# Kernel optimization log

Hardware: AMD Instinct MI355X
Metric: run time of the kernel (lower is better)

## Reference

```python
import jax, jax.numpy as jnp
import numpy as np

D0 = 1.0          # constraint distance d
NPEND = 128       # points per pendulum chain
NB = 1024         # number of chains (= batch.max()+1)
LATENT = 256      # latent dim of y
NDIM = 3          # spatial dimensions; x dim = 2*NDIM (pos + vel)


def setup_inputs() -> dict:
    key = jax.random.key(0)
    k1, k2, k3 = jax.random.split(key, 3)
    N = NB * NPEND
    y = jax.random.normal(k1, (N, LATENT), dtype=jnp.float32)
    z = jax.random.normal(k2, (N,), dtype=jnp.float32)
    K = jax.random.normal(k3, (LATENT, 2 * NDIM), dtype=jnp.float32) * 0.05
    batch = (jnp.arange(N, dtype=jnp.int32) // NPEND).astype(jnp.int32)
    return {"y": y, "z": z, "K": K, "batch": batch}


def _delta_r(r):
    # dr[:,0] = r[:,0]; dr[:,i] = r[:,i] - r[:,i-1]
    return jnp.concatenate([r[:, :1], r[:, 1:] - r[:, :-1]], axis=1)


def reference(y, z, K, batch):
    x = y @ K                                  # [N, 6]
    ndim = x.shape[-1] // 2                    # pos_only=False -> 3
    nb = batch.shape[0] // NPEND               # == batch.max()+1 by construction
    r = x[:, :ndim].reshape(nb, -1, ndim)      # [nb, npend, 3]

    dr = _delta_r(r)                           # [nb, npend, 3]
    drnorm = jnp.linalg.norm(dr, axis=-1)      # [nb, npend]
    c = drnorm - D0                            # constraint values
    rn = dr / drnorm[..., None]                # unit chain-difference vectors

    # Jacobian-transpose times constraints, fused over the chain dimension:
    # out[:,i] = c_i * rn_i - c_{i+1} * rn_{i+1};  out[:,-1] = c_{-1} * rn_{-1}
    t = c[..., None] * rn                      # [nb, npend, 3]
    out = t - jnp.concatenate([t[:, 1:], jnp.zeros_like(t[:, :1])], axis=1)

    lam_x = jnp.zeros_like(x).at[:, :ndim].set(out.reshape(-1, ndim))
    lam_y = lam_x @ K.T                        # [N, latent]
    return lam_y
```

## Files before the change

kernel.cpp:

```cpp
#include <hip/hip_runtime.h>

#define NPEND  128
#define LATENT 256
#define KCOLS  6
#define D0_C   1.0f
#define SEG    32
#define SEGS_PER_CHAIN (NPEND / SEG)
#define ROWS_PER_HALF 5

__global__ __launch_bounds__(256, 4)
void pend_kernel_f32(const float* __restrict__ y,
                     const float* __restrict__ K,
                     float* __restrict__ out)
{
    __shared__ float sKT[3][LATENT];
    __shared__ float sR[SEG + 2][3];

    const int tid  = threadIdx.x;
    const int hwid = tid >> 5;
    const int hl   = tid & 31;

    const int chain = blockIdx.x >> 2;
    const int seg   = blockIdx.x & 3;
    const int row0  = seg * SEG;
    const int rlo   = (row0 > 0) ? row0 - 1 : 0;
    const int rhi   = (row0 + SEG < NPEND) ? row0 + SEG : NPEND - 1;
    const int nrows = rhi - rlo + 1;

    {
        const float ka = K[tid * KCOLS + 0];
        const float kb = K[tid * KCOLS + 1];
        const float kc = K[tid * KCOLS + 2];
        sKT[0][tid] = ka;
        sKT[1][tid] = kb;
        sKT[2][tid] = kc;
    }
    __syncthreads();

    const size_t cbase = (size_t)chain * ((size_t)NPEND * LATENT);
    const int l0 = hl * 4;

    float4 va[ROWS_PER_HALF], vb[ROWS_PER_HALF];
#pragma unroll
    for (int j = 0; j < ROWS_PER_HALF; ++j) {
        int i = hwid + 8 * j;
        int row = rlo + ((i < nrows) ? i : (nrows - 1));
        const float* yr = y + cbase + (size_t)row * LATENT;
        va[j] = *(const float4*)(yr + l0);
        vb[j] = *(const float4*)(yr + 128 + l0);
    }

    const float4 k0a = *(const float4*)&sKT[0][l0];
    const float4 k0b = *(const float4*)&sKT[0][l0 + 128];
    const float4 k1a = *(const float4*)&sKT[1][l0];
    const float4 k1b = *(const float4*)&sKT[1][l0 + 128];
    const float4 k2a = *(const float4*)&sKT[2][l0];
    const float4 k2b = *(const float4*)&sKT[2][l0 + 128];

    __builtin_amdgcn_sched_barrier(0);

    float s0[ROWS_PER_HALF], s1[ROWS_PER_HALF], s2[ROWS_PER_HALF];
#pragma unroll
    for (int j = 0; j < ROWS_PER_HALF; ++j) {
        s0[j] = va[j].x*k0a.x + va[j].y*k0a.y + va[j].z*k0a.z + va[j].w*k0a.w
              + vb[j].x*k0b.x + vb[j].y*k0b.y + vb[j].z*k0b.z + vb[j].w*k0b.w;
        s1[j] = va[j].x*k1a.x + va[j].y*k1a.y + va[j].z*k1a.z + va[j].w*k1a.w
              + vb[j].x*k1b.x + vb[j].y*k1b.y + vb[j].z*k1b.z + vb[j].w*k1b.w;
        s2[j] = va[j].x*k2a.x + va[j].y*k2a.y + va[j].z*k2a.z + va[j].w*k2a.w
              + vb[j].x*k2b.x + vb[j].y*k2b.y + vb[j].z*k2b.z + vb[j].w*k2b.w;
    }

#pragma unroll
    for (int off = 16; off > 0; off >>= 1) {
#pragma unroll
        for (int j = 0; j < ROWS_PER_HALF; ++j) {
            s0[j] += __shfl_down(s0[j], off, 32);
            s1[j] += __shfl_down(s1[j], off, 32);
            s2[j] += __shfl_down(s2[j], off, 32);
        }
    }
    if (hl == 0) {
#pragma unroll
        for (int j = 0; j < ROWS_PER_HALF; ++j) {
            int i = hwid + 8 * j;
            if (i < nrows) {
                sR[i][0] = s0[j]; sR[i][1] = s1[j]; sR[i][2] = s2[j];
            }
        }
    }
    __syncthreads();

#pragma unroll
    for (int j = 0; j < SEG / 8; ++j) {
        const int i   = hwid + 8 * j;
        const int row = row0 + i;
        const int si  = row - rlo;

        const float rx = sR[si][0], ry = sR[si][1], rz = sR[si][2];
        float px = 0.f, py = 0.f, pz = 0.f;
        if (row > 0) { px = sR[si-1][0]; py = sR[si-1][1]; pz = sR[si-1][2]; }

        const float dx = rx - px, dy = ry - py, dz = rz - pz;
        const float n  = sqrtf(dx*dx + dy*dy + dz*dz);
        const float s  = (n - D0_C) / n;
        float ox = s * dx, oy = s * dy, oz = s * dz;

        if (row < NPEND - 1) {
            const float nx = sR[si+1][0], ny = sR[si+1][1], nz = sR[si+1][2];
            const float ex = nx - rx, ey = ny - ry, ez = nz - rz;
            const float n2 = sqrtf(ex*ex + ey*ey + ez*ez);
            const float t2 = (n2 - D0_C) / n2;
            ox -= t2 * ex; oy -= t2 * ey; oz -= t2 * ez;
        }

        float4 wa, wb;
        wa.x = ox*k0a.x + oy*k1a.x + oz*k2a.x;
        wa.y = ox*k0a.y + oy*k1a.y + oz*k2a.y;
        wa.z = ox*k0a.z + oy*k1a.z + oz*k2a.z;
        wa.w = ox*k0a.w + oy*k1a.w + oz*k2a.w;
        wb.x = ox*k0b.x + oy*k1b.x + oz*k2b.x;
        wb.y = ox*k0b.y + oy*k1b.y + oz*k2b.y;
        wb.z = ox*k0b.z + oy*k1b.z + oz*k2b.z;
        wb.w = ox*k0b.w + oy*k1b.w + oz*k2b.w;

        float* orow = out + cbase + (size_t)row * LATENT;
        *(float4*)(orow + l0)       = wa;
        *(float4*)(orow + 128 + l0) = wb;
    }
}

extern "C" void kernel_launch(void* const* d_in, const int* in_sizes, int n_in,
                              void* d_out, int out_size, void* d_ws, size_t ws_size,
                              hipStream_t stream) {
    const float* y = (const float*)d_in[0];
    const float* K = (const float*)d_in[2];
    float* out = (float*)d_out;

    int N  = (n_in > 1 && in_sizes) ? in_sizes[1] : (1024 * NPEND);
    int nb = N / NPEND;
    if (nb <= 0) nb = 1024;
    (void)out_size; (void)d_ws; (void)ws_size;

    pend_kernel_f32<<<nb * SEGS_PER_CHAIN, 256, 0, stream>>>(y, K, out);
}
```

Baseline: 236.0 us.

## Process whole chain per block with double-buffered segment loads

Each block now handles an entire 128-row chain instead of a 32-row segment, which removes the halo rows that were re-read from y at segment boundaries. Loads for the next segment are issued while the current segment is reduced, and each segment's output is written one iteration later so loads, reductions and stores overlap. Stores become nontemporal. In exchange the grid shrinks to 1024 blocks, which lowers parallelism, and register pressure rises from the double-buffered loads.

```diff
diff --git a/kernel.cpp b/kernel.cpp
--- a/kernel.cpp
+++ b/kernel.cpp
@@ -5,8 +5,10 @@
 #define KCOLS  6
 #define D0_C   1.0f
 #define SEG    32
-#define SEGS_PER_CHAIN (NPEND / SEG)
-#define ROWS_PER_HALF 5
+#define NSEG   (NPEND / SEG)
+#define JROWS  4
+
+typedef float f32x4 __attribute__((ext_vector_type(4)));
 
 __global__ __launch_bounds__(256, 4)
 void pend_kernel_f32(const float* __restrict__ y,
@@ -14,18 +16,15 @@
                      float* __restrict__ out)
 {
     __shared__ float sKT[3][LATENT];
-    __shared__ float sR[SEG + 2][3];
+    __shared__ float sR[NPEND][3];
 
     const int tid  = threadIdx.x;
     const int hwid = tid >> 5;
     const int hl   = tid & 31;
+    const int l0   = hl * 4;
 
-    const int chain = blockIdx.x >> 2;
-    const int seg   = blockIdx.x & 3;
-    const int row0  = seg * SEG;
-    const int rlo   = (row0 > 0) ? row0 - 1 : 0;
-    const int rhi   = (row0 + SEG < NPEND) ? row0 + SEG : NPEND - 1;
-    const int nrows = rhi - rlo + 1;
+    const int chain = blockIdx.x;
+    const size_t cbase = (size_t)chain * ((size_t)NPEND * LATENT);
 
     {
         const float ka = K[tid * KCOLS + 0];
@@ -37,19 +36,6 @@
     }
     __syncthreads();
 
-    const size_t cbase = (size_t)chain * ((size_t)NPEND * LATENT);
-    const int l0 = hl * 4;
-
-    float4 va[ROWS_PER_HALF], vb[ROWS_PER_HALF];
-#pragma unroll
-    for (int j = 0; j < ROWS_PER_HALF; ++j) {
-        int i = hwid + 8 * j;
-        int row = rlo + ((i < nrows) ? i : (nrows - 1));
-        const float* yr = y + cbase + (size_t)row * LATENT;
-        va[j] = *(const float4*)(yr + l0);
-        vb[j] = *(const float4*)(yr + 128 + l0);
-    }
-
     const float4 k0a = *(const float4*)&sKT[0][l0];
     const float4 k0b = *(const float4*)&sKT[0][l0 + 128];
     const float4 k1a = *(const float4*)&sKT[1][l0];
@@ -57,76 +43,96 @@
     const float4 k2a = *(const float4*)&sKT[2][l0];
     const float4 k2b = *(const float4*)&sKT[2][l0 + 128];
 
-    __builtin_amdgcn_sched_barrier(0);
+    float4 va[2][JROWS], vb[2][JROWS];
 
-    float s0[ROWS_PER_HALF], s1[ROWS_PER_HALF], s2[ROWS_PER_HALF];
+    auto issue = [&](int s, int b) {
 #pragma unroll
-    for (int j = 0; j < ROWS_PER_HALF; ++j) {
-        s0[j] = va[j].x*k0a.x + va[j].y*k0a.y + va[j].z*k0a.z + va[j].w*k0a.w
-              + vb[j].x*k0b.x + vb[j].y*k0b.y + vb[j].z*k0b.z + vb[j].w*k0b.w;
-        s1[j] = va[j].x*k1a.x + va[j].y*k1a.y + va[j].z*k1a.z + va[j].w*k1a.w
-              + vb[j].x*k1b.x + vb[j].y*k1b.y + vb[j].z*k1b.z + vb[j].w*k1b.w;
-        s2[j] = va[j].x*k2a.x + va[j].y*k2a.y + va[j].z*k2a.z + va[j].w*k2a.w
-              + vb[j].x*k2b.x + vb[j].y*k2b.y + vb[j].z*k2b.z + vb[j].w*k2b.w;
-    }
+        for (int j = 0; j < JROWS; ++j) {
+            const int row = s * SEG + hwid + 8 * j;
+            const float* yr = y + cbase + (size_t)row * LATENT;
+            va[b][j] = *(const float4*)(yr + l0);
+            vb[b][j] = *(const float4*)(yr + 128 + l0);
+        }
+    };
 
+    auto computeR = [&](int s, int b) {
+        float s0[JROWS], s1[JROWS], s2[JROWS];
 #pragma unroll
-    for (int off = 16; off > 0; off >>= 1) {
+        for (int j = 0; j < JROWS; ++j) {
+            const float4 a = va[b][j], bb = vb[b][j];
+            s0[j] = a.x*k0a.x + a.y*k0a.y + a.z*k0a.z + a.w*k0a.w
+                  + bb.x*k0b.x + bb.y*k0b.y + bb.z*k0b.z + bb.w*k0b.w;
+            s1[j] = a.x*k1a.x + a.y*k1a.y + a.z*k1a.z + a.w*k1a.w
+                  + bb.x*k1b.x + bb.y*k1b.y + bb.z*k1b.z + bb.w*k1b.w;
+            s2[j] = a.x*k2a.x + a.y*k2a.y + a.z*k2a.z + a.w*k2a.w
+                  + bb.x*k2b.x + bb.y*k2b.y + bb.z*k2b.z + bb.w*k2b.w;
+        }
 #pragma unroll
-        for (int j = 0; j < ROWS_PER_HALF; ++j) {
-            s0[j] += __shfl_down(s0[j], off, 32);
-            s1[j] += __shfl_down(s1[j], off, 32);
-            s2[j] += __shfl_down(s2[j], off, 32);
-        }
-    }
-    if (hl == 0) {
+        for (int off = 16; off > 0; off >>= 1) {
 #pragma unroll
-        for (int j = 0; j < ROWS_PER_HALF; ++j) {
-            int i = hwid + 8 * j;
-            if (i < nrows) {
-                sR[i][0] = s0[j]; sR[i][1] = s1[j]; sR[i][2] = s2[j];
+            for (int j = 0; j < JROWS; ++j) {
+                s0[j] += __shfl_down(s0[j], off, 32);
+                s1[j] += __shfl_down(s1[j], off, 32);
+                s2[j] += __shfl_down(s2[j], off, 32);
             }
         }
+        if (hl == 0) {
+#pragma unroll
+            for (int j = 0; j < JROWS; ++j) {
+                const int row = s * SEG + hwid + 8 * j;
+                sR[row][0] = s0[j]; sR[row][1] = s1[j]; sR[row][2] = s2[j];
+            }
+        }
+    };
+
+    auto phase2 = [&](int t) {
+#pragma unroll
+        for (int j = 0; j < JROWS; ++j) {
+            const int row = t * SEG + hwid + 8 * j;
+
+            const float rx = sR[row][0], ry = sR[row][1], rz = sR[row][2];
+            float px = 0.f, py = 0.f, pz = 0.f;
+            if (row > 0) { px = sR[row-1][0]; py = sR[row-1][1]; pz = sR[row-1][2]; }
+
+            const float dx = rx - px, dy = ry - py, dz = rz - pz;
+            const float n  = sqrtf(dx*dx + dy*dy + dz*dz);
+            const float s  = (n - D0_C) / n;
+            float ox = s * dx, oy = s * dy, oz = s * dz;
+
+            if (row < NPEND - 1) {
+                const float nx = sR[row+1][0], ny = sR[row+1][1], nz = sR[row+1][2];
+                const float ex = nx - rx, ey = ny - ry, ez = nz - rz;
+                const float n2 = sqrtf(ex*ex + ey*ey + ez*ez);
+                const float t2 = (n2 - D0_C) / n2;
+                ox -= t2 * ex; oy -= t2 * ey; oz -= t2 * ez;
+            }
+
+            f32x4 wa, wb;
+            wa.x = ox*k0a.x + oy*k1a.x + oz*k2a.x;
+            wa.y = ox*k0a.y + oy*k1a.y + oz*k2a.y;
+            wa.z = ox*k0a.z + oy*k1a.z + oz*k2a.z;
+            wa.w = ox*k0a.w + oy*k1a.w + oz*k2a.w;
+            wb.x = ox*k0b.x + oy*k1b.x + oz*k2b.x;
+            wb.y = ox*k0b.y + oy*k1b.y + oz*k2b.y;
+            wb.z = ox*k0b.z + oy*k1b.z + oz*k2b.z;
+            wb.w = ox*k0b.w + oy*k1b.w + oz*k2b.w;
+
+            float* orow = out + cbase + (size_t)row * LATENT;
+            __builtin_nontemporal_store(wa, (f32x4*)(orow + l0));
+            __builtin_nontemporal_store(wb, (f32x4*)(orow + 128 + l0));
+        }
+    };
+
+    issue(0, 0);
+#pragma unroll
+    for (int s = 0; s < NSEG; ++s) {
+        if (s + 1 < NSEG) issue(s + 1, (s + 1) & 1);
+        __builtin_amdgcn_sched_barrier(0);
+        computeR(s, s & 1);
+        __syncthreads();
+        if (s > 0) phase2(s - 1);
     }
-    __syncthreads();
-
-#pragma unroll
-    for (int j = 0; j < SEG / 8; ++j) {
-        const int i   = hwid + 8 * j;
-        const int row = row0 + i;
-        const int si  = row - rlo;
-
-        const float rx = sR[si][0], ry = sR[si][1], rz = sR[si][2];
-        float px = 0.f, py = 0.f, pz = 0.f;
-        if (row > 0) { px = sR[si-1][0]; py = sR[si-1][1]; pz = sR[si-1][2]; }
-
-        const float dx = rx - px, dy = ry - py, dz = rz - pz;
-        const float n  = sqrtf(dx*dx + dy*dy + dz*dz);
-        const float s  = (n - D0_C) / n;
-        float ox = s * dx, oy = s * dy, oz = s * dz;
-
-        if (row < NPEND - 1) {
-            const float nx = sR[si+1][0], ny = sR[si+1][1], nz = sR[si+1][2];
-            const float ex = nx - rx, ey = ny - ry, ez = nz - rz;
-            const float n2 = sqrtf(ex*ex + ey*ey + ez*ez);
-            const float t2 = (n2 - D0_C) / n2;
-            ox -= t2 * ex; oy -= t2 * ey; oz -= t2 * ez;
-        }
-
-        float4 wa, wb;
-        wa.x = ox*k0a.x + oy*k1a.x + oz*k2a.x;
-        wa.y = ox*k0a.y + oy*k1a.y + oz*k2a.y;
-        wa.z = ox*k0a.z + oy*k1a.z + oz*k2a.z;
-        wa.w = ox*k0a.w + oy*k1a.w + oz*k2a.w;
-        wb.x = ox*k0b.x + oy*k1b.x + oz*k2b.x;
-        wb.y = ox*k0b.y + oy*k1b.y + oz*k2b.y;
-        wb.z = ox*k0b.z + oy*k1b.z + oz*k2b.z;
-        wb.w = ox*k0b.w + oy*k1b.w + oz*k2b.w;
-
-        float* orow = out + cbase + (size_t)row * LATENT;
-        *(float4*)(orow + l0)       = wa;
-        *(float4*)(orow + 128 + l0) = wb;
-    }
+    phase2(NSEG - 1);
 }
 
 extern "C" void kernel_launch(void* const* d_in, const int* in_sizes, int n_in,
@@ -141,5 +147,5 @@
     if (nb <= 0) nb = 1024;
     (void)out_size; (void)d_ws; (void)ws_size;
 
-    pend_kernel_f32<<<nb * SEGS_PER_CHAIN, 256, 0, stream>>>(y, K, out);
+    pend_kernel_f32<<<nb, 256, 0, stream>>>(y, K, out);
 }
```

New measurement: 245.4 us. +4.0%, slower.

## Split into projection and output kernels to avoid reading halo rows twice

Applied to the files above, without the earlier changes.

Replaces the single fused kernel with two. The first is a persistent-style kernel that projects each row of y onto the first three columns of K, keeping K in registers, and writes the results to a global scratch buffer. The second reads those projected positions per segment, applies the constraint math and writes the output using nontemporal stores. The intent is to stop re-reading halo rows of y in every segment block and to keep output writes from polluting the cache, at the cost of an extra launch and a global round trip. The batch size is now capped at a fixed static buffer size.

```diff
diff --git a/kernel.cpp b/kernel.cpp
--- a/kernel.cpp
+++ b/kernel.cpp
@@ -4,27 +4,81 @@
 #define LATENT 256
 #define KCOLS  6
 #define D0_C   1.0f
-#define SEG    32
-#define SEGS_PER_CHAIN (NPEND / SEG)
-#define ROWS_PER_HALF 5
+#define NB_MAX 1024
+
+typedef float f32x4 __attribute__((ext_vector_type(4)));
+
+static __device__ float4 g_r[(size_t)NB_MAX * NPEND];
 
 __global__ __launch_bounds__(256, 4)
-void pend_kernel_f32(const float* __restrict__ y,
-                     const float* __restrict__ K,
+void pend_r_kernel(const float* __restrict__ y,
+                   const float* __restrict__ K,
+                   int ngroups)
+{
+    const int tid  = threadIdx.x;
+    const int lane = tid & 63;
+    const int g    = lane >> 4;
+    const int sl   = lane & 15;
+    const int k0   = sl * 16;
+
+    float kf0[16], kf1[16], kf2[16];
+#pragma unroll
+    for (int i = 0; i < 16; ++i) {
+        kf0[i] = K[(k0 + i) * KCOLS + 0];
+        kf1[i] = K[(k0 + i) * KCOLS + 1];
+        kf2[i] = K[(k0 + i) * KCOLS + 2];
+    }
+
+    const int wid    = (blockIdx.x << 2) | (tid >> 6);
+    const int wcount = gridDim.x << 2;
+
+    for (int grp = wid; grp < ngroups; grp += wcount) {
+        const int row = (grp << 2) + g;
+        const float* yr = y + (size_t)row * LATENT + k0;
+        const float4 a0 = *(const float4*)(yr + 0);
+        const float4 a1 = *(const float4*)(yr + 4);
+        const float4 a2 = *(const float4*)(yr + 8);
+        const float4 a3 = *(const float4*)(yr + 12);
+
+        const float av[16] = { a0.x, a0.y, a0.z, a0.w,
+                               a1.x, a1.y, a1.z, a1.w,
+                               a2.x, a2.y, a2.z, a2.w,
+                               a3.x, a3.y, a3.z, a3.w };
+        float s0 = 0.f, s1 = 0.f, s2 = 0.f;
+#pragma unroll
+        for (int i = 0; i < 16; ++i) {
+            s0 += av[i] * kf0[i];
+            s1 += av[i] * kf1[i];
+            s2 += av[i] * kf2[i];
+        }
+
+#pragma unroll
+        for (int off = 8; off >= 1; off >>= 1) {
+            s0 += __shfl_xor(s0, off, 16);
+            s1 += __shfl_xor(s1, off, 16);
+            s2 += __shfl_xor(s2, off, 16);
+        }
+        if (sl == 0) g_r[row] = make_float4(s0, s1, s2, 0.f);
+    }
+}
+
+__global__ __launch_bounds__(256, 8)
+void pend_out_kernel(const float* __restrict__ K,
                      float* __restrict__ out)
 {
-    __shared__ float sKT[3][LATENT];
-    __shared__ float sR[SEG + 2][3];
+    __shared__ float  sKT[3][LATENT];
+    __shared__ float4 sRr[36];
 
     const int tid  = threadIdx.x;
     const int hwid = tid >> 5;
     const int hl   = tid & 31;
+    const int l0   = hl * 4;
 
     const int chain = blockIdx.x >> 2;
     const int seg   = blockIdx.x & 3;
-    const int row0  = seg * SEG;
+    const int row0  = seg * 32;
     const int rlo   = (row0 > 0) ? row0 - 1 : 0;
-    const int rhi   = (row0 + SEG < NPEND) ? row0 + SEG : NPEND - 1;
+    const int rhi   = (row0 + 32 < NPEND) ? row0 + 32 : NPEND - 1;
     const int nrows = rhi - rlo + 1;
 
     {
@@ -35,20 +89,8 @@
         sKT[1][tid] = kb;
         sKT[2][tid] = kc;
     }
+    if (tid < nrows) sRr[tid] = g_r[chain * NPEND + rlo + tid];
     __syncthreads();
-
-    const size_t cbase = (size_t)chain * ((size_t)NPEND * LATENT);
-    const int l0 = hl * 4;
-
-    float4 va[ROWS_PER_HALF], vb[ROWS_PER_HALF];
-#pragma unroll
-    for (int j = 0; j < ROWS_PER_HALF; ++j) {
-        int i = hwid + 8 * j;
-        int row = rlo + ((i < nrows) ? i : (nrows - 1));
-        const float* yr = y + cbase + (size_t)row * LATENT;
-        va[j] = *(const float4*)(yr + l0);
-        vb[j] = *(const float4*)(yr + 128 + l0);
-    }
 
     const float4 k0a = *(const float4*)&sKT[0][l0];
     const float4 k0b = *(const float4*)&sKT[0][l0 + 128];
@@ -57,48 +99,18 @@
     const float4 k2a = *(const float4*)&sKT[2][l0];
     const float4 k2b = *(const float4*)&sKT[2][l0 + 128];
 
-    __builtin_amdgcn_sched_barrier(0);
-
-    float s0[ROWS_PER_HALF], s1[ROWS_PER_HALF], s2[ROWS_PER_HALF];
-#pragma unroll
-    for (int j = 0; j < ROWS_PER_HALF; ++j) {
-        s0[j] = va[j].x*k0a.x + va[j].y*k0a.y + va[j].z*k0a.z + va[j].w*k0a.w
-              + vb[j].x*k0b.x + vb[j].y*k0b.y + vb[j].z*k0b.z + vb[j].w*k0b.w;
-        s1[j] = va[j].x*k1a.x + va[j].y*k1a.y + va[j].z*k1a.z + va[j].w*k1a.w
-              + vb[j].x*k1b.x + vb[j].y*k1b.y + vb[j].z*k1b.z + vb[j].w*k1b.w;
-        s2[j] = va[j].x*k2a.x + va[j].y*k2a.y + va[j].z*k2a.z + va[j].w*k2a.w
-              + vb[j].x*k2b.x + vb[j].y*k2b.y + vb[j].z*k2b.z + vb[j].w*k2b.w;
-    }
+    const size_t cbase = (size_t)chain * ((size_t)NPEND * LATENT);
 
 #pragma unroll
-    for (int off = 16; off > 0; off >>= 1) {
-#pragma unroll
-        for (int j = 0; j < ROWS_PER_HALF; ++j) {
-            s0[j] += __shfl_down(s0[j], off, 32);
-            s1[j] += __shfl_down(s1[j], off, 32);
-            s2[j] += __shfl_down(s2[j], off, 32);
-        }
-    }
-    if (hl == 0) {
-#pragma unroll
-        for (int j = 0; j < ROWS_PER_HALF; ++j) {
-            int i = hwid + 8 * j;
-            if (i < nrows) {
-                sR[i][0] = s0[j]; sR[i][1] = s1[j]; sR[i][2] = s2[j];
-            }
-        }
-    }
-    __syncthreads();
-
-#pragma unroll
-    for (int j = 0; j < SEG / 8; ++j) {
+    for (int j = 0; j < 4; ++j) {
         const int i   = hwid + 8 * j;
         const int row = row0 + i;
         const int si  = row - rlo;
 
-        const float rx = sR[si][0], ry = sR[si][1], rz = sR[si][2];
+        const float4 rc = sRr[si];
+        const float rx = rc.x, ry = rc.y, rz = rc.z;
         float px = 0.f, py = 0.f, pz = 0.f;
-        if (row > 0) { px = sR[si-1][0]; py = sR[si-1][1]; pz = sR[si-1][2]; }
+        if (row > 0) { const float4 rp = sRr[si - 1]; px = rp.x; py = rp.y; pz = rp.z; }
 
         const float dx = rx - px, dy = ry - py, dz = rz - pz;
         const float n  = sqrtf(dx*dx + dy*dy + dz*dz);
@@ -106,14 +118,14 @@
         float ox = s * dx, oy = s * dy, oz = s * dz;
 
         if (row < NPEND - 1) {
-            const float nx = sR[si+1][0], ny = sR[si+1][1], nz = sR[si+1][2];
-            const float ex = nx - rx, ey = ny - ry, ez = nz - rz;
+            const float4 rn = sRr[si + 1];
+            const float ex = rn.x - rx, ey = rn.y - ry, ez = rn.z - rz;
             const float n2 = sqrtf(ex*ex + ey*ey + ez*ez);
             const float t2 = (n2 - D0_C) / n2;
             ox -= t2 * ex; oy -= t2 * ey; oz -= t2 * ez;
         }
 
-        float4 wa, wb;
+        f32x4 wa, wb;
         wa.x = ox*k0a.x + oy*k1a.x + oz*k2a.x;
         wa.y = ox*k0a.y + oy*k1a.y + oz*k2a.y;
         wa.z = ox*k0a.z + oy*k1a.z + oz*k2a.z;
@@ -124,8 +136,8 @@
         wb.w = ox*k0b.w + oy*k1b.w + oz*k2b.w;
 
         float* orow = out + cbase + (size_t)row * LATENT;
-        *(float4*)(orow + l0)       = wa;
-        *(float4*)(orow + 128 + l0) = wb;
+        __builtin_nontemporal_store(wa, (f32x4*)(orow + l0));
+        __builtin_nontemporal_store(wb, (f32x4*)(orow + 128 + l0));
     }
 }
 
@@ -139,7 +151,11 @@
     int N  = (n_in > 1 && in_sizes) ? in_sizes[1] : (1024 * NPEND);
     int nb = N / NPEND;
     if (nb <= 0) nb = 1024;
+    if (nb > NB_MAX) nb = NB_MAX;
+    N = nb * NPEND;
     (void)out_size; (void)d_ws; (void)ws_size;
 
-    pend_kernel_f32<<<nb * SEGS_PER_CHAIN, 256, 0, stream>>>(y, K, out);
+    const int ngroups = N / 4;
+    pend_r_kernel<<<2048, 256, 0, stream>>>(y, K, ngroups);
+    pend_out_kernel<<<nb * 4, 256, 0, stream>>>(K, out);
 }
```

New measurement: 245.8 us. 4.2% more time.
